# Kernel optimization log

Measured on AMD Instinct MI355X. Metric: run time of the kernel, lower is better.

The kernel has to match this reference:

```python
import jax, jax.numpy as jnp
import numpy as np

VMF_KAPPA = 30.0      # vMF concentration
THRESHOLD = 0.0       # vc_thresholds
OCC_LIKELY = 0.6      # occ_likely[0]
NUM_MIXTURES = 4
EPS_L1 = 1e-12        # torch F.normalize eps


def _l1_normalize(x, axis):
    n = jnp.sum(jnp.abs(x), axis=axis, keepdims=True)
    return x / jnp.maximum(n, EPS_L1)


def _crop_or_pad(mm, H, W):
    # center crop or zero-pad mix model spatial dims to (H, W); shapes are static
    _, _, hm, wm = mm.shape
    if hm < H:
        d1 = (H - hm) // 2
        mm = jnp.pad(mm, ((0, 0), (0, 0), (d1, H - hm - d1), (0, 0)))
    elif hm > H:
        d1 = (hm - H) // 2
        mm = mm[:, :, d1:d1 + H, :]
    if wm < W:
        d1 = (W - wm) // 2
        mm = jnp.pad(mm, ((0, 0), (0, 0), (0, 0), (d1, W - wm - d1)))
    elif wm > W:
        d1 = (wm - W) // 2
        mm = mm[:, :, :, d1:d1 + W]
    return mm


def setup_inputs() -> dict:
    key = jax.random.key(0)
    k1, k2, k3, k4 = jax.random.split(key, 4)
    B, C, H, W = 32, 512, 56, 56
    VC = 512              # number of vMF codebook vectors
    KM = 48               # num_classes(12) * num_mixtures(4)
    NCLUT = 5             # clutter models
    return {
        "vgg_feat": jax.random.normal(k1, (B, C, H, W), dtype=jnp.float32),
        "conv_weight": jax.random.normal(k2, (VC, C, 1, 1), dtype=jnp.float32),
        "mix_model": jax.random.uniform(k3, (KM, VC, H, W), dtype=jnp.float32),
        "clutter_model": jax.random.uniform(k4, (NCLUT, VC), dtype=jnp.float32),
    }


def reference(vgg_feat, conv_weight, mix_model, clutter_model):
    B, C, H, W = vgg_feat.shape
    # --- Conv1o1: cosine similarity between L2-normalized features and codebook ---
    xnorm = jnp.linalg.norm(vgg_feat, axis=1, keepdims=True)
    xnorm = xnorm + (xnorm == 0).astype(vgg_feat.dtype)  # avoid div-by-zero
    xn = vgg_feat / xnorm
    w = conv_weight[:, :, 0, 0]                           # (vc, C) 1x1 kernel
    wn = w / jnp.linalg.norm(w, axis=1, keepdims=True)
    cos = jnp.einsum('bchw,kc->bkhw', xn, wn)             # (B, vc, H, W)
    # --- vMF activation ---
    act = jnp.exp(VMF_KAPPA * cos) * (cos > THRESHOLD).astype(cos.dtype)
    # --- PointwiseInferenceLayer (vmf, use_mixture_bg=True) ---
    ck = _l1_normalize(jnp.clip(clutter_model, 0.0, 1.0), axis=1)  # (N, vc)
    bg = jnp.einsum('bkhw,nk->bnhw', act, ck)                      # (B, N, H, W)
    background = jnp.log(bg * OCC_LIKELY + 1e-10)
    background = jnp.max(background, axis=1, keepdims=True)        # (B, 1, H, W)
    background = background[:, None, None]                         # (B,1,1,1,H,W)

    mm = _l1_normalize(jnp.clip(mix_model, 0.0, 1.0), axis=1)      # (KM, vc, Hm, Wm)
    mm = _crop_or_pad(mm, H, W)
    fg = jnp.einsum('bkhw,mkhw->bmhw', act, mm)                    # (B, KM, H, W)
    foreground = jnp.log(fg * (1.0 - OCC_LIKELY) + 1e-10)
    num_classes = mm.shape[0] // NUM_MIXTURES
    foreground = foreground.reshape(B, num_classes, NUM_MIXTURES, 1, H, W)
    per_model = jnp.maximum(foreground, background).sum(axis=(-1, -2))  # (B,K,M,1)
    scores = per_model.max(axis=-1).max(axis=-1)                        # (B, K)
    mix_likeli = scores / (H * W)
    # SoftMaxTemp(2.0)
    z = jnp.exp(jnp.clip(mix_likeli * 2.0, -88.7, 88.7))
    soft = z / jnp.sum(z, axis=1, keepdims=True)
    return soft, vgg_feat, mix_likeli
```

## Files before the change

### kernel.cpp

```cpp
#include <hip/hip_runtime.h>

#define B_ 32
#define C_ 512
#define HW_ 3136
#define KF_ 512
#define KM_ 48
#define NCL_ 5

typedef __attribute__((ext_vector_type(8))) short short8;
typedef __attribute__((ext_vector_type(4))) short short4v;
typedef __attribute__((ext_vector_type(4))) float floatx4;
typedef unsigned int u32;
typedef u32 __attribute__((address_space(1))) gu32;
typedef u32 __attribute__((address_space(3))) lu32;

__device__ __forceinline__ unsigned short f2bf(float f) {
    union { float f; unsigned u; } v; v.f = f;
    unsigned r = v.u + 0x7FFFu + ((v.u >> 16) & 1u);
    return (unsigned short)(r >> 16);
}
__device__ __forceinline__ void gl2lds16(const void* g, void* l) {
    __builtin_amdgcn_global_load_lds((const gu32*)g, (lu32*)l, 16, 0, 0);
}

__global__ __launch_bounds__(64) void prep_kernel(const float* __restrict__ w,
                                                  const float* __restrict__ cl,
                                                  unsigned short* __restrict__ wn,
                                                  float* __restrict__ ck) {
    int bid = blockIdx.x, t = threadIdx.x;
    if (bid < KF_) {
        const float* row = w + (size_t)bid * C_;
        float ss = 0.f;
        float x[8];
#pragma unroll
        for (int j = 0; j < 8; ++j) { x[j] = row[t * 8 + j]; ss += x[j] * x[j]; }
        for (int m = 32; m >= 1; m >>= 1) ss += __shfl_xor(ss, m);
        float inv = 1.f / sqrtf(ss);
#pragma unroll
        for (int j = 0; j < 8; ++j) wn[(size_t)bid * C_ + t * 8 + j] = f2bf(x[j] * inv);
    } else {
        int n = bid - KF_;
        if (n >= NCL_) return;
        const float* row = cl + (size_t)n * KF_;
        float s = 0.f;
        float v[8];
#pragma unroll
        for (int j = 0; j < 8; ++j) {
            float x = row[t * 8 + j];
            x = fminf(fmaxf(x, 0.f), 1.f);
            v[j] = x; s += x;
        }
        for (int m = 32; m >= 1; m >>= 1) s += __shfl_xor(s, m);
        float inv = 1.f / fmaxf(s, 1e-12f);
#pragma unroll
        for (int j = 0; j < 8; ++j) ck[(size_t)n * KF_ + t * 8 + j] = v[j] * inv;
    }
}

__global__ __launch_bounds__(512) void xprep_kernel(const float* __restrict__ vgg,
                                                    unsigned short* __restrict__ xnt,
                                                    float* __restrict__ invn,
                                                    float* __restrict__ out_vgg,
                                                    int write_vgg) {
    int pt = blockIdx.x, b = blockIdx.y;
    int tid = threadIdx.x;
    int px = tid & 63, cq = tid >> 6;
    __shared__ __align__(16) unsigned short tile[64][512];
    __shared__ float ssp[8][64];
    const float* vcol = vgg + (size_t)b * C_ * HW_ + pt * 64 + px;
    float* ovcol = out_vgg + (size_t)b * C_ * HW_ + pt * 64 + px;

    float ss = 0.f;
#pragma unroll
    for (int j = 0; j < 16; ++j) {
        int c0 = cq * 64 + j * 4;
        float x0 = vcol[(size_t)(c0 + 0) * HW_];
        float x1 = vcol[(size_t)(c0 + 1) * HW_];
        float x2 = vcol[(size_t)(c0 + 2) * HW_];
        float x3 = vcol[(size_t)(c0 + 3) * HW_];
        ss += x0 * x0 + x1 * x1 + x2 * x2 + x3 * x3;
        short4v pk;
        pk[0] = (short)f2bf(x0); pk[1] = (short)f2bf(x1);
        pk[2] = (short)f2bf(x2); pk[3] = (short)f2bf(x3);
        *(short4v*)&tile[px][c0] = pk;
        if (write_vgg) {
            ovcol[(size_t)(c0 + 0) * HW_] = x0;
            ovcol[(size_t)(c0 + 1) * HW_] = x1;
            ovcol[(size_t)(c0 + 2) * HW_] = x2;
            ovcol[(size_t)(c0 + 3) * HW_] = x3;
        }
    }
    ssp[cq][px] = ss;
    __syncthreads();
    if (tid < 64) {
        float s = 0.f;
#pragma unroll
        for (int q = 0; q < 8; ++q) s += ssp[q][tid];
        float n = sqrtf(s);
        invn[(size_t)b * HW_ + pt * 64 + tid] = (n == 0.f) ? 1.f : 1.f / n;
    }
    __syncthreads();
    int row = tid >> 3, ch = tid & 7;
    unsigned short* orow = xnt + ((size_t)b * HW_ + pt * 64 + row) * 512;
#pragma unroll
    for (int j = 0; j < 8; ++j) {
        int c8 = (ch + 8 * j) * 8;
        *(short8*)(orow + c8) = *(const short8*)&tile[row][c8];
    }
}

__global__ __launch_bounds__(512) void gemm_act_kernel(const unsigned short* __restrict__ xnt,
                                                       const unsigned short* __restrict__ wn,
                                                       const float* __restrict__ invn,
                                                       const float* __restrict__ ck,
                                                       unsigned short* __restrict__ act,
                                                       float* __restrict__ bgacc) {
    int wg = blockIdx.x;
    int swz = (wg & 7) * 392 + (wg >> 3);
    int pt = swz >> 2, ft = swz & 3;
    int tid = threadIdx.x, lane = tid & 63;
    int wid = tid >> 6;
    int li = lane & 15, q = lane >> 4;
    int wm = wid & 1, wq = wid >> 1;

    __shared__ __align__(16) unsigned short a_lds[2][128 * 64];
    __shared__ __align__(16) unsigned short b_lds[2][128 * 64];
    __shared__ float inv_l[128];
    __shared__ float ck_l[NCL_ * KF_];
    __shared__ float bga_l[128 * NCL_];
    if (tid < 128) inv_l[tid] = invn[(size_t)pt * 128 + tid];
    for (int i = tid; i < NCL_ * KF_; i += 512) ck_l[i] = ck[i];
    for (int i = tid; i < 128 * NCL_; i += 512) bga_l[i] = 0.f;

    const unsigned short* ga = wn + ((size_t)ft * 128 + (tid >> 3)) * 512 + (tid & 7) * 8;
    const unsigned short* gb = xnt + ((size_t)pt * 128 + (tid >> 3)) * 512 + (tid & 7) * 8;
    int ldst = tid * 8;

    floatx4 acc[4][2] = {};

#pragma unroll
    for (int i = 0; i < 2; ++i) {
        gl2lds16(ga + (size_t)i * 64 * 512, &a_lds[0][ldst + i * 4096]);
        gl2lds16(gb + (size_t)i * 64 * 512, &b_lds[0][ldst + i * 4096]);
    }

#pragma unroll 1
    for (int s = 0; s < 8; ++s) {
        __builtin_amdgcn_s_barrier();
        if (s < 7) {
            int nb = (s + 1) & 1;
#pragma unroll
            for (int i = 0; i < 2; ++i) {
                gl2lds16(ga + (size_t)i * 64 * 512 + (s + 1) * 64, &a_lds[nb][ldst + i * 4096]);
                gl2lds16(gb + (size_t)i * 64 * 512 + (s + 1) * 64, &b_lds[nb][ldst + i * 4096]);
            }
            asm volatile("s_waitcnt vmcnt(4)" ::: "memory");
        } else {
            asm volatile("s_waitcnt vmcnt(0)" ::: "memory");
        }
        __builtin_amdgcn_sched_barrier(0);
        __builtin_amdgcn_s_barrier();
        int buf = s & 1;
#pragma unroll
        for (int k2 = 0; k2 < 2; ++k2) {
            short8 af[4], bfr[2];
#pragma unroll
            for (int i = 0; i < 4; ++i)
                af[i] = *(const short8*)&a_lds[buf][(wm * 64 + i * 16 + li) * 64 + k2 * 32 + q * 8];
#pragma unroll
            for (int j = 0; j < 2; ++j)
                bfr[j] = *(const short8*)&b_lds[buf][(wq * 32 + j * 16 + li) * 64 + k2 * 32 + q * 8];
#pragma unroll
            for (int i = 0; i < 4; ++i)
#pragma unroll
                for (int j = 0; j < 2; ++j)
                    acc[i][j] = __builtin_amdgcn_mfma_f32_16x16x32_bf16(af[i], bfr[j], acc[i][j], 0, 0, 0);
        }
    }

#pragma unroll
    for (int j = 0; j < 2; ++j) {
        int px = wq * 32 + j * 16 + li;
        float inv = inv_l[px];
        size_t row_g = (size_t)pt * 128 + px;
        float bp[NCL_] = {0.f, 0.f, 0.f, 0.f, 0.f};
#pragma unroll
        for (int i = 0; i < 4; ++i) {
            int chn = ft * 8 + wm * 4 + i;
            int f_g = ft * 128 + wm * 64 + i * 16 + q * 4;
            short4v pk;
            float av[4];
#pragma unroll
            for (int r = 0; r < 4; ++r) {
                float cv = acc[i][j][r] * inv;
                float a = cv > 0.f ? __expf(30.f * cv) : 0.f;
                av[r] = a;
                pk[r] = (short)f2bf(a);
            }
            *(short4v*)(act + ((size_t)chn * 100352 + row_g) * 16 + q * 4) = pk;
#pragma unroll
            for (int n = 0; n < NCL_; ++n)
                bp[n] += av[0] * ck_l[n * KF_ + f_g] + av[1] * ck_l[n * KF_ + f_g + 1] +
                         av[2] * ck_l[n * KF_ + f_g + 2] + av[3] * ck_l[n * KF_ + f_g + 3];
        }
#pragma unroll
        for (int n = 0; n < NCL_; ++n) {
            float v = bp[n];
            v += __shfl_xor(v, 16);
            v += __shfl_xor(v, 32);
            if (q == 0) atomicAdd(&bga_l[px * NCL_ + n], v);
        }
    }
    __syncthreads();
    if (tid < 128) {
        size_t row_g = (size_t)pt * 128 + tid;
#pragma unroll
        for (int n = 0; n < NCL_; ++n)
            atomicAdd(&bgacc[row_g * 8 + n], bga_l[tid * NCL_ + n]);
    }
}

#define FG4_MML 0
#define FG4_ACTL 32768
#define FG4_BGS 65536
#define FG4_CSUM 67584
#define FG4_PMS 69632
__global__ __launch_bounds__(512, 4) void fg4_kernel(const unsigned short* __restrict__ act,
                                                     const float* __restrict__ mm,
                                                     const float* __restrict__ bgacc,
                                                     float* __restrict__ pm) {
    __shared__ __align__(16) unsigned char L[70656];
    float* bgs    = (float*)(L + FG4_BGS);
    float* csum_s = (float*)(L + FG4_CSUM);
    float* pms    = (float*)(L + FG4_PMS);

    int bid = blockIdx.x;
    int xcd = bid & 7, pos = bid >> 3;
    int linear = (xcd < 4 ? xcd * 74 : 296 + (xcd - 4) * 73) + pos;
    int pt = linear / 6, sub = linear - pt * 6;
    int mg = sub >> 1, bh = sub & 1;
    int p0 = pt * 32, m0 = mg * 16, b0 = bh * 16;

    int tid = threadIdx.x;
    int lane = tid & 63, w = tid >> 6;
    int li = lane & 15, q = lane >> 4;

    if (tid < 256) pms[tid] = 0.f;
    csum_s[tid] = 0.f;
    {
        int b = tid >> 5, px = tid & 31;
        const float* bgp = bgacc + ((size_t)(b0 + b) * HW_ + p0 + px) * 8;
        float mx = -1e30f;
#pragma unroll
        for (int n = 0; n < NCL_; ++n) mx = fmaxf(mx, logf(bgp[n] * 0.6f + 1e-10f));
        bgs[b * 32 + px] = mx;
    }

    int ab = tid >> 5, apx = tid & 31;
    int mmM = tid >> 5, mkq = (tid >> 3) & 3, mpxg = tid & 7;
    const unsigned short* aSrc = act + ((size_t)(b0 + ab) * HW_ + p0 + apx) * 16;
    const float* mSrc = mm + ((size_t)(m0 + mmM) * KF_ + mkq * 4) * HW_ + p0 + mpxg * 4;
    unsigned char* aW = L + FG4_ACTL + ab * 1024 + ((apx ^ (ab & 3)) * 32);

    floatx4 mr[4];
    short8 ar[2];
    float cs[4] = {0.f, 0.f, 0.f, 0.f};
    floatx4 acc[4] = {};
    short8 fa[4], fb[4];

    auto loadRegs = [&](int s) {
#pragma unroll
        for (int j = 0; j < 4; ++j)
            mr[j] = *(const floatx4*)(mSrc + ((size_t)s * 16 + j) * HW_);
        const unsigned short* as = aSrc + (size_t)s * 1605632;
        ar[0] = *(const short8*)(as);
        ar[1] = *(const short8*)(as + 8);
    };
    auto cvtWrite = [&](int s) {
        int buf = (s & 1) * 16384;
#pragma unroll
        for (int i = 0; i < 4; ++i) {
            int px = mpxg * 4 + i;
            float x0 = fminf(fmaxf(mr[0][i], 0.f), 1.f);
            float x1 = fminf(fmaxf(mr[1][i], 0.f), 1.f);
            float x2 = fminf(fmaxf(mr[2][i], 0.f), 1.f);
            float x3 = fminf(fmaxf(mr[3][i], 0.f), 1.f);
            cs[i] += x0 + x1 + x2 + x3;
            short4v pk;
            pk[0] = (short)f2bf(x0); pk[1] = (short)f2bf(x1);
            pk[2] = (short)f2bf(x2); pk[3] = (short)f2bf(x3);
            *(short4v*)(L + FG4_MML + buf + mmM * 1024 + ((px ^ (mmM & 3)) * 32) + mkq * 8) = pk;
        }
        *(short8*)(aW + buf) = ar[0];
        *(short8*)(aW + buf + 16) = ar[1];
    };

    loadRegs(0);
    cvtWrite(0);
    loadRegs(1);
    __syncthreads();

#pragma unroll 2
    for (int s = 0; s < 32; ++s) {
        const unsigned char* bufM = L + FG4_MML + (s & 1) * 16384;
        const unsigned char* bufA = L + FG4_ACTL + (s & 1) * 16384;
        if ((q >> 1) == (s & 1)) {
#pragma unroll
            for (int e = 0; e < 4; ++e) {
                int px = w * 4 + e;
                int off = li * 1024 + ((px ^ (li & 3)) * 32) + (q & 1) * 16;
                fa[e] = *(const short8*)(bufM + off);
                fb[e] = *(const short8*)(bufA + off);
            }
        }
        if (s & 1) {
#pragma unroll
            for (int e = 0; e < 4; ++e)
                acc[e] = __builtin_amdgcn_mfma_f32_16x16x32_bf16(fa[e], fb[e], acc[e], 0, 0, 0);
        }
        if (s < 31) {
            cvtWrite(s + 1);
            if (s < 30) loadRegs(s + 2);
        }
        __syncthreads();
    }

#pragma unroll
    for (int i = 0; i < 4; ++i)
        atomicAdd(&csum_s[mmM * 32 + mpxg * 4 + i], cs[i]);
    __syncthreads();

#pragma unroll
    for (int r = 0; r < 4; ++r) {
        int m = q * 4 + r;
        float sacc = 0.f;
#pragma unroll
        for (int e = 0; e < 4; ++e) {
            int px = w * 4 + e;
            float inv = 1.f / fmaxf(csum_s[m * 32 + px], 1e-12f);
            float v = fmaxf(logf(acc[e][r] * inv * 0.4f + 1e-10f), bgs[li * 32 + px]);
            sacc += v;
        }
        atomicAdd(&pms[m * 16 + li], sacc);
    }
    __syncthreads();
    if (tid < 256) {
        int m = tid >> 4, b = tid & 15;
        atomicAdd(&pm[(size_t)(b0 + b) * KM_ + m0 + m], pms[m * 16 + b]);
    }
}

__global__ __launch_bounds__(64) void final_kernel(const float* __restrict__ pm,
                                                   float* __restrict__ out_soft,
                                                   float* __restrict__ out_ml) {
    int b = threadIdx.x;
    if (b >= B_) return;
    float ml[12];
#pragma unroll
    for (int c = 0; c < 12; ++c) {
        float s = -1e30f;
#pragma unroll
        for (int j = 0; j < 4; ++j) s = fmaxf(s, pm[(size_t)b * KM_ + c * 4 + j]);
        ml[c] = s / (float)HW_;
    }
    float z[12], zs = 0.f;
#pragma unroll
    for (int c = 0; c < 12; ++c) {
        float e = fminf(fmaxf(ml[c] * 2.f, -88.7f), 88.7f);
        z[c] = expf(e); zs += z[c];
    }
#pragma unroll
    for (int c = 0; c < 12; ++c) {
        out_soft[(size_t)b * 12 + c] = z[c] / zs;
        out_ml[(size_t)b * 12 + c] = ml[c];
    }
}

extern "C" void kernel_launch(void* const* d_in, const int* in_sizes, int n_in,
                              void* d_out, int out_size, void* d_ws, size_t ws_size,
                              hipStream_t stream) {
    const float* vgg = (const float*)d_in[0];
    const float* cw  = (const float*)d_in[1];
    const float* mmp = (const float*)d_in[2];
    const float* cl  = (const float*)d_in[3];
    float* out = (float*)d_out;
    char* ws = (char*)d_ws;

    unsigned short* wn   = (unsigned short*)(ws);
    float* ck            = (float*)(ws + 524288);
    float* invn          = (float*)(ws + 534528);
    float* pm            = (float*)(ws + 935936);
    float* bgacc         = (float*)(ws + 942080);
    unsigned short* xnt  = (unsigned short*)(ws + 4153344);
    const size_t ACT_OFF = 4153344 + 102760448;
    const size_t ACT_BYTES = (size_t)B_ * HW_ * KF_ * 2;

    int act_in_ws = (ws_size >= ACT_OFF + ACT_BYTES) ? 1 : 0;
    unsigned short* act = act_in_ws ? (unsigned short*)(ws + ACT_OFF)
                                    : (unsigned short*)(out + 384);

    hipMemsetAsync(pm, 0, (size_t)B_ * KM_ * sizeof(float), stream);
    hipMemsetAsync(bgacc, 0, (size_t)B_ * HW_ * 8 * sizeof(float), stream);
    prep_kernel<<<dim3(KF_ + NCL_), dim3(64), 0, stream>>>(cw, cl, wn, ck);
    xprep_kernel<<<dim3(49, 32), dim3(512), 0, stream>>>(vgg, xnt, invn, out + 384, act_in_ws);
    gemm_act_kernel<<<dim3(3136), dim3(512), 0, stream>>>(xnt, wn, invn, ck, act, bgacc);
    fg4_kernel<<<dim3(588), dim3(512), 0, stream>>>(act, mmp, bgacc, pm);
    final_kernel<<<1, 64, 0, stream>>>(pm, out, out + 384 + (size_t)B_ * C_ * HW_);
    if (!act_in_ws)
        hipMemcpyAsync(out + 384, vgg, (size_t)B_ * C_ * HW_ * sizeof(float),
                       hipMemcpyDeviceToDevice, stream);
}
```

Measured before the change: 402.2 us.

## Load fg activations via direct global-to-LDS and deepen mix-model prefetch pipeline

Activation tiles in the foreground kernel are now copied straight from global memory into LDS with global_load_lds instead of passing through registers. The mix-model register prefetch is double-slotted, so loads run three stages ahead. The single barrier moves to the top of the loop and uses explicit vmcnt/lgkmcnt waits. The goal is more memory latency hidden behind the MFMA work and lower register pressure, at the cost of hand-tuned waitcnt logic that must match the number of loads in flight.

```diff
diff --git a/kernel.cpp b/kernel.cpp
--- a/kernel.cpp
+++ b/kernel.cpp
@@ -220,19 +220,19 @@
     }
 }
 
-#define FG4_MML 0
-#define FG4_ACTL 32768
-#define FG4_BGS 65536
-#define FG4_CSUM 67584
-#define FG4_PMS 69632
-__global__ __launch_bounds__(512, 4) void fg4_kernel(const unsigned short* __restrict__ act,
+#define FG5_MML 0
+#define FG5_ACTL 32768
+#define FG5_BGS 65536
+#define FG5_CSUM 67584
+#define FG5_PMS 69632
+__global__ __launch_bounds__(512, 4) void fg5_kernel(const unsigned short* __restrict__ act,
                                                      const float* __restrict__ mm,
                                                      const float* __restrict__ bgacc,
                                                      float* __restrict__ pm) {
     __shared__ __align__(16) unsigned char L[70656];
-    float* bgs    = (float*)(L + FG4_BGS);
-    float* csum_s = (float*)(L + FG4_CSUM);
-    float* pms    = (float*)(L + FG4_PMS);
+    float* bgs    = (float*)(L + FG5_BGS);
+    float* csum_s = (float*)(L + FG5_CSUM);
+    float* pms    = (float*)(L + FG5_PMS);
 
     int bid = blockIdx.x;
     int xcd = bid & 7, pos = bid >> 3;
@@ -255,55 +255,74 @@
         for (int n = 0; n < NCL_; ++n) mx = fmaxf(mx, logf(bgp[n] * 0.6f + 1e-10f));
         bgs[b * 32 + px] = mx;
     }
-
-    int ab = tid >> 5, apx = tid & 31;
+    __syncthreads();
+
+    const unsigned short* aS[2];
+    int aD[2];
+#pragma unroll
+    for (int t = 0; t < 2; ++t) {
+        int b = w * 2 + t;
+        aS[t] = act + ((size_t)(b0 + b) * HW_ + p0 + ((lane >> 1) ^ (b & 3))) * 16 + (lane & 1) * 8;
+        aD[t] = FG5_ACTL + b * 1024 + lane * 16;
+    }
+
     int mmM = tid >> 5, mkq = (tid >> 3) & 3, mpxg = tid & 7;
-    const unsigned short* aSrc = act + ((size_t)(b0 + ab) * HW_ + p0 + apx) * 16;
     const float* mSrc = mm + ((size_t)(m0 + mmM) * KF_ + mkq * 4) * HW_ + p0 + mpxg * 4;
-    unsigned char* aW = L + FG4_ACTL + ab * 1024 + ((apx ^ (ab & 3)) * 32);
-
-    floatx4 mr[4];
-    short8 ar[2];
+
+    floatx4 mr[2][4];
     float cs[4] = {0.f, 0.f, 0.f, 0.f};
     floatx4 acc[4] = {};
     short8 fa[4], fb[4];
 
-    auto loadRegs = [&](int s) {
+    auto issueAct = [&](int s) {
+        int buf = (s & 1) * 16384;
+        size_t co = (size_t)s * 1605632;
+#pragma unroll
+        for (int t = 0; t < 2; ++t)
+            gl2lds16(aS[t] + co, L + aD[t] + buf);
+    };
+    auto loadRegs = [&](int s, int slot) {
 #pragma unroll
         for (int j = 0; j < 4; ++j)
-            mr[j] = *(const floatx4*)(mSrc + ((size_t)s * 16 + j) * HW_);
-        const unsigned short* as = aSrc + (size_t)s * 1605632;
-        ar[0] = *(const short8*)(as);
-        ar[1] = *(const short8*)(as + 8);
+            mr[slot][j] = *(const floatx4*)(mSrc + ((size_t)s * 16 + j) * HW_);
     };
     auto cvtWrite = [&](int s) {
         int buf = (s & 1) * 16384;
+        int slot = s & 1;
 #pragma unroll
         for (int i = 0; i < 4; ++i) {
             int px = mpxg * 4 + i;
-            float x0 = fminf(fmaxf(mr[0][i], 0.f), 1.f);
-            float x1 = fminf(fmaxf(mr[1][i], 0.f), 1.f);
-            float x2 = fminf(fmaxf(mr[2][i], 0.f), 1.f);
-            float x3 = fminf(fmaxf(mr[3][i], 0.f), 1.f);
+            float x0 = fminf(fmaxf(mr[slot][0][i], 0.f), 1.f);
+            float x1 = fminf(fmaxf(mr[slot][1][i], 0.f), 1.f);
+            float x2 = fminf(fmaxf(mr[slot][2][i], 0.f), 1.f);
+            float x3 = fminf(fmaxf(mr[slot][3][i], 0.f), 1.f);
             cs[i] += x0 + x1 + x2 + x3;
             short4v pk;
             pk[0] = (short)f2bf(x0); pk[1] = (short)f2bf(x1);
             pk[2] = (short)f2bf(x2); pk[3] = (short)f2bf(x3);
-            *(short4v*)(L + FG4_MML + buf + mmM * 1024 + ((px ^ (mmM & 3)) * 32) + mkq * 8) = pk;
-        }
-        *(short8*)(aW + buf) = ar[0];
-        *(short8*)(aW + buf + 16) = ar[1];
+            *(short4v*)(L + FG5_MML + buf + mmM * 1024 + ((px ^ (mmM & 3)) * 32) + mkq * 8) = pk;
+        }
     };
 
-    loadRegs(0);
+    issueAct(0);
+    loadRegs(0, 0);
+    loadRegs(1, 1);
     cvtWrite(0);
-    loadRegs(1);
-    __syncthreads();
+    loadRegs(2, 0);
 
 #pragma unroll 2
     for (int s = 0; s < 32; ++s) {
-        const unsigned char* bufM = L + FG4_MML + (s & 1) * 16384;
-        const unsigned char* bufA = L + FG4_ACTL + (s & 1) * 16384;
+        if (s <= 29) asm volatile("s_waitcnt vmcnt(4) lgkmcnt(0)" ::: "memory");
+        else         asm volatile("s_waitcnt vmcnt(0) lgkmcnt(0)" ::: "memory");
+        __builtin_amdgcn_sched_barrier(0);
+        __builtin_amdgcn_s_barrier();
+        if (s < 31) {
+            issueAct(s + 1);
+            cvtWrite(s + 1);
+            if (s + 3 < 32) loadRegs(s + 3, (s + 3) & 1);
+        }
+        const unsigned char* bufM = L + FG5_MML + (s & 1) * 16384;
+        const unsigned char* bufA = L + FG5_ACTL + (s & 1) * 16384;
         if ((q >> 1) == (s & 1)) {
 #pragma unroll
             for (int e = 0; e < 4; ++e) {
@@ -318,11 +337,6 @@
             for (int e = 0; e < 4; ++e)
                 acc[e] = __builtin_amdgcn_mfma_f32_16x16x32_bf16(fa[e], fb[e], acc[e], 0, 0, 0);
         }
-        if (s < 31) {
-            cvtWrite(s + 1);
-            if (s < 30) loadRegs(s + 2);
-        }
-        __syncthreads();
     }
 
 #pragma unroll
@@ -404,7 +418,7 @@
     prep_kernel<<<dim3(KF_ + NCL_), dim3(64), 0, stream>>>(cw, cl, wn, ck);
     xprep_kernel<<<dim3(49, 32), dim3(512), 0, stream>>>(vgg, xnt, invn, out + 384, act_in_ws);
     gemm_act_kernel<<<dim3(3136), dim3(512), 0, stream>>>(xnt, wn, invn, ck, act, bgacc);
-    fg4_kernel<<<dim3(588), dim3(512), 0, stream>>>(act, mmp, bgacc, pm);
+    fg5_kernel<<<dim3(588), dim3(512), 0, stream>>>(act, mmp, bgacc, pm);
     final_kernel<<<1, 64, 0, stream>>>(pm, out, out + 384 + (size_t)B_ * C_ * HW_);
     if (!act_in_ws)
         hipMemcpyAsync(out + 384, vgg, (size_t)B_ * C_ * HW_ * sizeof(float),
```

Result: slower. 428.7 us (+6.6%).
